# Kernel optimization log

Hardware: AMD Instinct MI355X
Metric: run time of the kernel (lower is better)

## Reference

```python
import jax, jax.numpy as jnp
import numpy as np

B, N, K = 16, 8192, 16
H1, H3 = 512, 64
EPS = 1e-5


def _bn(x, g, b):
    # BatchNorm1d training-mode math: normalize per-channel (last axis) over all other axes.
    ax = tuple(range(x.ndim - 1))
    m = x.mean(ax, keepdims=True)
    v = x.var(ax, keepdims=True)  # biased variance, as in torch BN forward
    return (x - m) * jax.lax.rsqrt(v + EPS) * g + b


def _gather(h, idx):
    # h: [b,n,f], idx: [b,n,k] -> [b,n,k,f] per-batch neighbor gather
    return jax.vmap(lambda hb, ib: hb[ib])(h, idx)


def _forward(data, knn, e1_w, e1_b, e1_g, e1_be,
             gc1_w, gc1_b, g1_g, g1_be, gc2_w, gc2_b, g2_g, g2_be,
             e2_w, e2_b, e2_g, e2_be,
             d1_w, d1_b, d1_g, d1_be, d2_w, d2_b, d2_g, d2_be):
    b, n, _ = data.shape
    # local covariance features
    neigh = _gather(data, knn)                       # [b,n,K,3]
    cen = neigh - neigh.mean(axis=2, keepdims=True)
    cov = jnp.einsum('bnki,bnkj->bnij', cen, cen) / (K - 1)
    x = jnp.concatenate([data, cov.reshape(b, n, 9)], axis=-1)  # [b,n,12]
    # e_layers1: Linear(12,h3) + BN + ReLU
    x = jax.nn.relu(_bn(x @ e1_w + e1_b, e1_g, e1_be))
    # GCNConv over uniform-degree kNN graph with self loop: (h_i + sum_j h_j)/(K+1)
    deg = float(K + 1)
    h = x @ gc1_w
    h = (h + _gather(h, knn).sum(axis=2)) / deg + gc1_b
    x = jax.nn.relu(_bn(h, g1_g, g1_be))
    h = x @ gc2_w
    h = (h + _gather(h, knn).sum(axis=2)) / deg + gc2_b
    x = jax.nn.relu(_bn(h, g2_g, g2_be))             # [b,n,h1]
    # AdaptiveMaxPool1d(1) over nodes
    x = x.max(axis=1, keepdims=True)                 # [b,1,h1]
    # e_layers2: Linear(h1,h1) + BN + ReLU
    x = jax.nn.relu(_bn(x @ e2_w + e2_b, e2_g, e2_be))
    # decode: folding grid
    nx_ = int(1 + (n * 120 / 60) ** 0.5)
    ny_ = int(1 + (n * 60 / 120) ** 0.5)
    xg = jnp.linspace(1.0, 120.0, nx_)
    yg = jnp.linspace(1.0, 60.0, ny_)
    grid = jnp.stack(jnp.meshgrid(xg, yg, indexing='ij'), axis=-1).reshape(-1, 2)[:n]
    kfeat = jnp.broadcast_to(x, (b, n, x.shape[-1]))  # codeword repeated per node
    y = jnp.broadcast_to(grid[None], (b, n, 2))
    z = jnp.concatenate([kfeat, y], axis=-1)          # [b,n,h1+2]
    z = jax.nn.relu(_bn(z @ d1_w + d1_b, d1_g, d1_be))
    z = jnp.concatenate([kfeat, z], axis=-1)          # [b,n,h1+3]
    z = jax.nn.relu(_bn(z @ d2_w + d2_b, d2_g, d2_be))
    return z                                          # [b,n,3]


def setup_inputs() -> dict:
    key = jax.random.key(0)
    ks = jax.random.split(key, 8)

    def lin(k, i, o):
        s = 1.0 / np.sqrt(i)
        return jax.random.uniform(k, (i, o), jnp.float32, -s, s)

    ones = lambda c: jnp.ones((c,), jnp.float32)
    zeros = lambda c: jnp.zeros((c,), jnp.float32)
    return {
        'data': jax.random.normal(ks[0], (B, N, 3), jnp.float32),
        'knn': jax.random.randint(ks[1], (B, N, K), 0, N),
        'e1_w': lin(ks[2], 12, H3), 'e1_b': zeros(H3), 'e1_g': ones(H3), 'e1_be': zeros(H3),
        'gc1_w': lin(ks[3], H3, 2 * H3), 'gc1_b': zeros(2 * H3), 'g1_g': ones(2 * H3), 'g1_be': zeros(2 * H3),
        'gc2_w': lin(ks[4], 2 * H3, H1), 'gc2_b': zeros(H1), 'g2_g': ones(H1), 'g2_be': zeros(H1),
        'e2_w': lin(ks[5], H1, H1), 'e2_b': zeros(H1), 'e2_g': ones(H1), 'e2_be': zeros(H1),
        'd1_w': lin(ks[6], H1 + 2, 3), 'd1_b': zeros(3), 'd1_g': ones(3), 'd1_be': zeros(3),
        'd2_w': lin(ks[7], H1 + 3, 3), 'd2_b': zeros(3), 'd2_g': ones(3), 'd2_be': zeros(3),
    }


def reference(data, knn, e1_w, e1_b, e1_g, e1_be,
              gc1_w, gc1_b, g1_g, g1_be, gc2_w, gc2_b, g2_g, g2_be,
              e2_w, e2_b, e2_g, e2_be,
              d1_w, d1_b, d1_g, d1_be, d2_w, d2_b, d2_g, d2_be):
    return _forward(data, knn, e1_w, e1_b, e1_g, e1_be,
                    gc1_w, gc1_b, g1_g, g1_be, gc2_w, gc2_b, g2_g, g2_be,
                    e2_w, e2_b, e2_g, e2_be,
                    d1_w, d1_b, d1_g, d1_be, d2_w, d2_b, d2_g, d2_be)
```

## Files before the change

kernel.cpp:

```cpp
#include <hip/hip_runtime.h>
#include <hip/hip_fp16.h>
#include <stdint.h>

#define BATCH 16
#define NPTS  8192
#define KNN   16
#define NROWS (BATCH*NPTS)
#define EPSBN 1e-5f
#define DEGINV (1.0f/17.0f)

typedef _Float16 f16x8 __attribute__((ext_vector_type(8)));
typedef float    f32x4 __attribute__((ext_vector_type(4)));

__device__ __forceinline__ unsigned short f2hu(float f) {
    union { _Float16 h; unsigned short u; } cv;
    cv.h = (_Float16)f;
    return cv.u;
}
__device__ __forceinline__ float hu2f(unsigned short u) {
    union { unsigned short u; _Float16 h; } cv;
    cv.u = u;
    return (float)cv.h;
}
__device__ __forceinline__ unsigned fenc(float f) {
    unsigned u = __float_as_uint(f);
    return (int)u >= 0 ? (u | 0x80000000u) : ~u;
}
__device__ __forceinline__ float fdec(unsigned k) {
    return (k & 0x80000000u) ? __uint_as_float(k & 0x7FFFFFFFu) : __uint_as_float(~k);
}

#define SZ_S1    0
#define SZ_S2P   128
#define SZ_S3P   16512
#define SZ_S4    82048
#define SZ_C1    83072
#define SZ_GN    83080
#define SZ_D2    83088
#define SZ_SCSH1 83096
#define SZ_SCSH2 83224
#define SZ_TOT   83480

__global__ __launch_bounds__(256) void k_prep(
    const float* __restrict__ gc1w, const float* __restrict__ gc2w,
    const float* __restrict__ d1w, const float* __restrict__ d1b,
    unsigned short* __restrict__ W1T, unsigned short* __restrict__ W2T,
    float* __restrict__ gn, float* __restrict__ statszone, unsigned* __restrict__ mm)
{
    int t = blockIdx.x * 256 + threadIdx.x;
    int NT_ = gridDim.x * 256;
    for (int i = t; i < 65536; i += NT_) {
        int c = i >> 7, k = i & 127;
        W2T[i] = f2hu(gc2w[k * 512 + c]);
    }
    for (int i = t; i < 8192; i += NT_) {
        int c = i >> 6, k = i & 63;
        W1T[i] = f2hu(gc1w[k * 128 + c]);
    }
    for (int i = t; i < SZ_TOT; i += NT_) statszone[i] = 0.f;
    for (int i = t; i < 8192; i += NT_) mm[i] = 0u;
    for (int i = t; i < 8192; i += NT_) mm[8192 + i] = 0xFFFFFFFFu;
    for (int n = t; n < 8192; n += NT_) {
        int ix = n / 65, iy = n % 65;
        float gx = 1.f + ix * (119.f / 128.f);
        float gy = 1.f + iy * (59.f / 64.f);
        #pragma unroll
        for (int j = 0; j < 3; j++)
            gn[n * 3 + j] = gx * d1w[512 * 3 + j] + gy * d1w[513 * 3 + j] + d1b[j];
    }
}

__global__ __launch_bounds__(256) void k_cov_e1(
    const float* __restrict__ data, const int* __restrict__ knn,
    const float* __restrict__ e1w, const float* __restrict__ e1b,
    unsigned short* __restrict__ a1)
{
    __shared__ float w[12 * 64];
    __shared__ float bias[64];
    int tid = threadIdx.x;
    for (int i = tid; i < 768; i += 256) w[i] = e1w[i];
    if (tid < 64) bias[tid] = e1b[tid];
    __syncthreads();

    int gid = blockIdx.x * 256 + tid;
    int b = gid >> 13;
    const float* db = data + (size_t)b * NPTS * 3;
    const int4* k4 = (const int4*)knn + gid * 4;

    float sx = 0, sy = 0, sz = 0, Sxx = 0, Sxy = 0, Sxz = 0, Syy = 0, Syz = 0, Szz = 0;
    #pragma unroll
    for (int jj = 0; jj < 4; jj++) {
        int4 q = k4[jj];
        int id[4] = {q.x, q.y, q.z, q.w};
        #pragma unroll
        for (int u = 0; u < 4; u++) {
            const float* p = db + (size_t)id[u] * 3;
            float x = p[0], y = p[1], z = p[2];
            sx += x; sy += y; sz += z;
            Sxx += x * x; Sxy += x * y; Sxz += x * z;
            Syy += y * y; Syz += y * z; Szz += z * z;
        }
    }
    float mx = sx * (1.f / 16.f), my = sy * (1.f / 16.f), mz = sz * (1.f / 16.f);
    const float inv15 = 1.f / 15.f;
    float x12[12];
    x12[0] = data[(size_t)gid * 3 + 0];
    x12[1] = data[(size_t)gid * 3 + 1];
    x12[2] = data[(size_t)gid * 3 + 2];
    x12[3] = (Sxx - 16.f * mx * mx) * inv15;
    x12[4] = (Sxy - 16.f * mx * my) * inv15;
    x12[5] = (Sxz - 16.f * mx * mz) * inv15;
    x12[6] = x12[4];
    x12[7] = (Syy - 16.f * my * my) * inv15;
    x12[8] = (Syz - 16.f * my * mz) * inv15;
    x12[9] = x12[5];
    x12[10] = x12[8];
    x12[11] = (Szz - 16.f * mz * mz) * inv15;

    unsigned short* arow = a1 + (size_t)gid * 64;
    for (int c0 = 0; c0 < 64; c0 += 8) {
        float v8[8];
        #pragma unroll
        for (int u = 0; u < 8; u++) {
            int c = c0 + u;
            float acc = bias[c];
            #pragma unroll
            for (int i = 0; i < 12; i++) acc += x12[i] * w[i * 64 + c];
            v8[u] = acc;
        }
        uint4 o;
        o.x = f2hu(v8[0]) | ((unsigned)f2hu(v8[1]) << 16);
        o.y = f2hu(v8[2]) | ((unsigned)f2hu(v8[3]) << 16);
        o.z = f2hu(v8[4]) | ((unsigned)f2hu(v8[5]) << 16);
        o.w = f2hu(v8[6]) | ((unsigned)f2hu(v8[7]) << 16);
        *(uint4*)(arow + c0) = o;
    }
}

__global__ __launch_bounds__(256) void k_reduce_a1(
    const unsigned short* __restrict__ a1, float* __restrict__ stats1)
{
    int tid = threadIdx.x;
    int c = tid & 63, rq = tid >> 6;
    float s = 0.f, q = 0.f;
    for (int row = blockIdx.x * 4 + rq; row < NROWS; row += gridDim.x * 4) {
        float v = hu2f(a1[(size_t)row * 64 + c]);
        s += v; q += v * v;
    }
    __shared__ float red[2][256];
    red[0][tid] = s; red[1][tid] = q;
    __syncthreads();
    if (tid < 64) {
        s = red[0][tid] + red[0][tid + 64] + red[0][tid + 128] + red[0][tid + 192];
        q = red[1][tid] + red[1][tid + 64] + red[1][tid + 128] + red[1][tid + 192];
        atomicAdd(stats1 + tid, s);
        atomicAdd(stats1 + 64 + tid, q);
    }
}

template <int C, int NPARTS>
__global__ __launch_bounds__(256) void k_bncoef(
    const float* __restrict__ statsIn,
    const float* __restrict__ gamma, const float* __restrict__ beta,
    float* __restrict__ scsh)
{
    int ch = threadIdx.x;
    if (ch < C) {
        float s = 0.f, q = 0.f;
        for (int p = 0; p < NPARTS; p++) {
            s += statsIn[p * 2 * C + ch];
            q += statsIn[p * 2 * C + C + ch];
        }
        float m = s * (1.f / NROWS);
        float var = fmaxf(q * (1.f / NROWS) - m * m, 0.f);
        float sc = gamma[ch] * rsqrtf(var + EPSBN);
        scsh[ch] = sc;
        scsh[C + ch] = beta[ch] - m * sc;
    }
}

template <int CIN>
__global__ __launch_bounds__(256) void k_gather16(
    const unsigned short* __restrict__ ain, const int* __restrict__ knn,
    const float* __restrict__ scsh, unsigned short* __restrict__ S)
{
    constexpr int GPR = CIN / 8;
    constexpr int R = 256 / GPR;
    constexpr int R2 = 2 * R;
    constexpr int BPB = NPTS / R2;

    __shared__ int nidx[R2 * KNN];

    int tid = threadIdx.x;
    int blk = blockIdx.x;
    int xcd = blk & 7;
    int idx = blk >> 3;
    int batch = xcd + 8 * (idx / BPB);
    int within = idx % BPB;
    int node0 = batch * NPTS + within * R2;

    {
        const int4* ksrc = (const int4*)(knn + (size_t)node0 * KNN);
        for (int i = tid; i < R2 * 4; i += 256) ((int4*)nidx)[i] = ksrc[i];
    }
    __syncthreads();

    int t = tid & (GPR - 1);
    int r0 = tid / GPR;
    int col8 = t * 8;
    float sc8[8], sh8[8];
    #pragma unroll
    for (int j = 0; j < 8; j++) { sc8[j] = scsh[col8 + j]; sh8[j] = scsh[CIN + col8 + j]; }

    int ra = node0 + r0;
    int rb = node0 + r0 + R;
    const unsigned short* abase = ain + (size_t)batch * NPTS * CIN;

    float acca[8], accb[8];
    {
        uint4 va = *(const uint4*)(ain + (size_t)ra * CIN + col8);
        uint4 vb = *(const uint4*)(ain + (size_t)rb * CIN + col8);
        unsigned wa[4] = {va.x, va.y, va.z, va.w};
        unsigned wb[4] = {vb.x, vb.y, vb.z, vb.w};
        #pragma unroll
        for (int j = 0; j < 4; j++) {
            acca[2*j]   = fmaxf(hu2f((unsigned short)(wa[j] & 0xFFFF)) * sc8[2*j]   + sh8[2*j],   0.f);
            acca[2*j+1] = fmaxf(hu2f((unsigned short)(wa[j] >> 16))    * sc8[2*j+1] + sh8[2*j+1], 0.f);
            accb[2*j]   = fmaxf(hu2f((unsigned short)(wb[j] & 0xFFFF)) * sc8[2*j]   + sh8[2*j],   0.f);
            accb[2*j+1] = fmaxf(hu2f((unsigned short)(wb[j] >> 16))    * sc8[2*j+1] + sh8[2*j+1], 0.f);
        }
    }
    #pragma unroll
    for (int jn = 0; jn < KNN; jn++) {
        int sa = nidx[r0 * KNN + jn];
        int sb = nidx[(r0 + R) * KNN + jn];
        uint4 va = *(const uint4*)(abase + (size_t)sa * CIN + col8);
        uint4 vb = *(const uint4*)(abase + (size_t)sb * CIN + col8);
        unsigned wa[4] = {va.x, va.y, va.z, va.w};
        unsigned wb[4] = {vb.x, vb.y, vb.z, vb.w};
        #pragma unroll
        for (int j = 0; j < 4; j++) {
            acca[2*j]   += fmaxf(hu2f((unsigned short)(wa[j] & 0xFFFF)) * sc8[2*j]   + sh8[2*j],   0.f);
            acca[2*j+1] += fmaxf(hu2f((unsigned short)(wa[j] >> 16))    * sc8[2*j+1] + sh8[2*j+1], 0.f);
            accb[2*j]   += fmaxf(hu2f((unsigned short)(wb[j] & 0xFFFF)) * sc8[2*j]   + sh8[2*j],   0.f);
            accb[2*j+1] += fmaxf(hu2f((unsigned short)(wb[j] >> 16))    * sc8[2*j+1] + sh8[2*j+1], 0.f);
        }
    }
    uint4 oa, ob;
    oa.x = f2hu(acca[0]) | ((unsigned)f2hu(acca[1]) << 16);
    oa.y = f2hu(acca[2]) | ((unsigned)f2hu(acca[3]) << 16);
    oa.z = f2hu(acca[4]) | ((unsigned)f2hu(acca[5]) << 16);
    oa.w = f2hu(acca[6]) | ((unsigned)f2hu(acca[7]) << 16);
    ob.x = f2hu(accb[0]) | ((unsigned)f2hu(accb[1]) << 16);
    ob.y = f2hu(accb[2]) | ((unsigned)f2hu(accb[3]) << 16);
    ob.z = f2hu(accb[4]) | ((unsigned)f2hu(accb[5]) << 16);
    ob.w = f2hu(accb[6]) | ((unsigned)f2hu(accb[7]) << 16);
    *(uint4*)(S + (size_t)ra * CIN + col8) = oa;
    *(uint4*)(S + (size_t)rb * CIN + col8) = ob;
}

template <int CIN, int COUT, int NSPLIT, bool STORE>
__global__ __launch_bounds__(256) void k_gemm(
    const unsigned short* __restrict__ S, const unsigned short* __restrict__ WT,
    const float* __restrict__ bias,
    unsigned short* __restrict__ aout, float* __restrict__ statsOut, unsigned* __restrict__ mm)
{
    constexpr int KC = CIN / 32;
    constexpr int MT = 128;
    constexpr int SST = CIN + 8;
    constexpr int CPB = COUT / NSPLIT;
    constexpr int CPW = CPB / 4;
    constexpr int NT = CPW / 16;

    __shared__ alignas(16) unsigned short sA[MT * SST];

    int tid = threadIdx.x;
    int blk = blockIdx.x;
    int xcd = blk & 7;
    int rest = blk >> 3;
    int nq = rest % NSPLIT;
    int mseq = rest / NSPLIT;
    int phase = mseq >> 6;
    int within = mseq & 63;
    int batch = xcd + 8 * phase;
    int node0 = batch * NPTS + within * MT;
    int cbase = nq * CPB;
    int pout = batch * 4 + (within >> 4);

    {
        constexpr int TOT = MT * CIN / 8;
        const uint4* src = (const uint4*)(S + (size_t)node0 * CIN);
        #pragma unroll
        for (int i = tid; i < TOT; i += 256) {
            int row = i / (CIN / 8);
            int col8 = (i % (CIN / 8)) * 8;
            *(uint4*)&sA[row * SST + col8] = src[i];
        }
    }
    __syncthreads();

    int lane = tid & 63, wv = tid >> 6;
    int n15 = lane & 15, qd = lane >> 4;
    int c0 = cbase + wv * CPW;

    f16x8 wf[KC][NT];
    float bz[NT];
    #pragma unroll
    for (int nt = 0; nt < NT; nt++) {
        int c = c0 + nt * 16 + n15;
        bz[nt] = bias[c];
        #pragma unroll
        for (int kc = 0; kc < KC; kc++)
            wf[kc][nt] = *(const f16x8*)(WT + (size_t)c * CIN + kc * 32 + qd * 8);
    }
    float sacc[NT], qacc[NT], mxa[NT], mna[NT];
    #pragma unroll
    for (int nt = 0; nt < NT; nt++) {
        sacc[nt] = 0.f; qacc[nt] = 0.f; mxa[nt] = -3.4e38f; mna[nt] = 3.4e38f;
    }

    #pragma unroll
    for (int mt = 0; mt < MT / 16; mt++) {
        f16x8 af[KC];
        #pragma unroll
        for (int kc = 0; kc < KC; kc++)
            af[kc] = *(const f16x8*)&sA[(mt * 16 + n15) * SST + kc * 32 + qd * 8];

        f32x4 acc[NT];
        #pragma unroll
        for (int nt = 0; nt < NT; nt++) acc[nt] = (f32x4)(0.f);
        #pragma unroll
        for (int kc = 0; kc < KC; kc++)
            #pragma unroll
            for (int nt = 0; nt < NT; nt++)
                acc[nt] = __builtin_amdgcn_mfma_f32_16x16x32_f16(af[kc], wf[kc][nt], acc[nt], 0, 0, 0);

        #pragma unroll
        for (int nt = 0; nt < NT; nt++) {
            int c = c0 + nt * 16 + n15;
            #pragma unroll
            for (int r = 0; r < 4; r++) {
                float a = acc[nt][r];
                sacc[nt] += a;
                qacc[nt] = fmaf(a, a, qacc[nt]);
                if (!STORE) {
                    mxa[nt] = fmaxf(mxa[nt], a);
                    mna[nt] = fminf(mna[nt], a);
                }
                if (STORE) {
                    float v = a * DEGINV + bz[nt];
                    int node = node0 + mt * 16 + qd * 4 + r;
                    aout[(size_t)node * COUT + c] = f2hu(v);
                }
            }
        }
    }

    #pragma unroll
    for (int nt = 0; nt < NT; nt++) {
        int c = c0 + nt * 16 + n15;
        float S_ = sacc[nt], Q_ = qacc[nt];
        S_ += __shfl_xor(S_, 16); S_ += __shfl_xor(S_, 32);
        Q_ += __shfl_xor(Q_, 16); Q_ += __shfl_xor(Q_, 32);
        if (!STORE) {
            float mx = mxa[nt], mn = mna[nt];
            mx = fmaxf(mx, __shfl_xor(mx, 16)); mx = fmaxf(mx, __shfl_xor(mx, 32));
            mn = fminf(mn, __shfl_xor(mn, 16)); mn = fminf(mn, __shfl_xor(mn, 32));
            if (lane < 16) {
                atomicMax(mm + batch * COUT + c, fenc(mx * DEGINV + bz[nt]));
                atomicMin(mm + BATCH * COUT + batch * COUT + c, fenc(mn * DEGINV + bz[nt]));
            }
        }
        if (lane < 16) {
            float b = bz[nt];
            float s = DEGINV * S_ + (float)MT * b;
            float q = DEGINV * DEGINV * Q_ + 2.f * DEGINV * b * S_ + (float)MT * b * b;
            atomicAdd(statsOut + (size_t)pout * 2 * COUT + c, s);
            atomicAdd(statsOut + (size_t)pout * 2 * COUT + COUT + c, q);
        }
    }
}

__global__ __launch_bounds__(256) void k_e2(
    const float* __restrict__ stats3p, const unsigned* __restrict__ mm,
    const float* __restrict__ g2g, const float* __restrict__ g2be,
    const float* __restrict__ e2w, const float* __restrict__ e2b,
    float* __restrict__ a4, float* __restrict__ stats4)
{
    __shared__ float pooled[512];
    int b = blockIdx.x, tid = threadIdx.x;
    for (int c = tid; c < 512; c += 256) {
        float s = 0.f, qq = 0.f;
        for (int p = 0; p < 64; p++) {
            s += stats3p[p * 1024 + c];
            qq += stats3p[p * 1024 + 512 + c];
        }
        float m = s * (1.f / NROWS);
        float var = fmaxf(qq * (1.f / NROWS) - m * m, 0.f);
        float sc = g2g[c] * rsqrtf(var + EPSBN);
        float sh = g2be[c] - m * sc;
        float amax = fdec(mm[b * 512 + c]);
        float amin = fdec(mm[8192 + b * 512 + c]);
        pooled[c] = fmaxf(fmaxf(sc * amax + sh, 0.f), fmaxf(sc * amin + sh, 0.f));
    }
    __syncthreads();
    int ca = tid, cb = tid + 256;
    float acc1 = e2b[ca], acc2 = e2b[cb];
    for (int f = 0; f < 512; f++) {
        float pv = pooled[f];
        acc1 += pv * e2w[f * 512 + ca];
        acc2 += pv * e2w[f * 512 + cb];
    }
    a4[b * 512 + ca] = acc1; a4[b * 512 + cb] = acc2;
    atomicAdd(stats4 + ca, acc1); atomicAdd(stats4 + 512 + ca, acc1 * acc1);
    atomicAdd(stats4 + cb, acc2); atomicAdd(stats4 + 512 + cb, acc2 * acc2);
}

__global__ __launch_bounds__(256) void k_code(
    const float* __restrict__ a4, const float* __restrict__ stats4,
    const float* __restrict__ e2g, const float* __restrict__ e2be,
    const float* __restrict__ d1w, const float* __restrict__ d2w,
    const float* __restrict__ gn,
    float* __restrict__ c1, float* __restrict__ c2,
    float* __restrict__ c1stats, float* __restrict__ gnstats)
{
    int b = blockIdx.x, tid = threadIdx.x;
    int lane = tid & 63, wv = tid >> 6;
    float p1[3] = {0, 0, 0}, p2[3] = {0, 0, 0};
    for (int c = tid; c < 512; c += 256) {
        float s = stats4[c], qq = stats4[512 + c];
        float m = s * (1.f / 16.f);
        float var = fmaxf(qq * (1.f / 16.f) - m * m, 0.f);
        float sc = e2g[c] * rsqrtf(var + EPSBN);
        float sh = e2be[c] - m * sc;
        float cv = fmaxf(sc * a4[b * 512 + c] + sh, 0.f);
        #pragma unroll
        for (int j = 0; j < 3; j++) {
            p1[j] += cv * d1w[c * 3 + j];
            p2[j] += cv * d2w[c * 3 + j];
        }
    }
    __shared__ float red[4][6];
    #pragma unroll
    for (int j = 0; j < 3; j++)
        for (int off = 32; off; off >>= 1) {
            p1[j] += __shfl_xor(p1[j], off);
            p2[j] += __shfl_xor(p2[j], off);
        }
    if (lane == 0) {
        #pragma unroll
        for (int j = 0; j < 3; j++) { red[wv][j] = p1[j]; red[wv][3 + j] = p2[j]; }
    }
    __syncthreads();
    if (tid < 3) {
        float v = red[0][tid] + red[1][tid] + red[2][tid] + red[3][tid];
        c1[b * 3 + tid] = v;
        atomicAdd(c1stats + tid, v);
        atomicAdd(c1stats + 3 + tid, v * v);
    } else if (tid < 6) {
        int j = tid - 3;
        float v = red[0][tid] + red[1][tid] + red[2][tid] + red[3][tid];
        c2[b * 3 + j] = v;
    }
    if (blockIdx.x == 0) {
        float g1[3] = {0, 0, 0}, g2s[3] = {0, 0, 0};
        for (int n = tid; n < NPTS; n += 256) {
            #pragma unroll
            for (int j = 0; j < 3; j++) {
                float g = gn[n * 3 + j];
                g1[j] += g; g2s[j] += g * g;
            }
        }
        #pragma unroll
        for (int j = 0; j < 3; j++)
            for (int off = 32; off; off >>= 1) {
                g1[j] += __shfl_xor(g1[j], off);
                g2s[j] += __shfl_xor(g2s[j], off);
            }
        __shared__ float redg[4][6];
        if (lane == 0) {
            #pragma unroll
            for (int j = 0; j < 3; j++) { redg[wv][j] = g1[j]; redg[wv][3 + j] = g2s[j]; }
        }
        __syncthreads();
        if (tid < 6)
            gnstats[tid] = redg[0][tid] + redg[1][tid] + redg[2][tid] + redg[3][tid];
    }
}

__device__ __forceinline__ void d1_coefs(
    const float* c1stats, const float* gnstats,
    const float* d1g, const float* d1be, float* scd, float* shd)
{
    #pragma unroll
    for (int j = 0; j < 3; j++) {
        float mc = c1stats[j] * (1.f / 16.f), qc = c1stats[3 + j] * (1.f / 16.f);
        float mg = gnstats[j] * (1.f / 8192.f), qg = gnstats[3 + j] * (1.f / 8192.f);
        float m = mc + mg;
        float var = fmaxf((qc - mc * mc) + (qg - mg * mg), 0.f);
        float sc = d1g[j] * rsqrtf(var + EPSBN);
        scd[j] = sc;
        shd[j] = d1be[j] - m * sc;
    }
}

__global__ __launch_bounds__(256) void k_d2stats(
    const float* __restrict__ c1, const float* __restrict__ c2, const float* __restrict__ gn,
    const float* __restrict__ c1stats, const float* __restrict__ gnstats,
    const float* __restrict__ d1g, const float* __restrict__ d1be,
    const float* __restrict__ d2w, const float* __restrict__ d2b,
    float* __restrict__ statsd2)
{
    int gid = blockIdx.x * 256 + threadIdx.x;
    int b = gid >> 13, n = gid & 8191;
    int lane = threadIdx.x & 63, wv = threadIdx.x >> 6;
    float scd[3], shd[3];
    d1_coefs(c1stats, gnstats, d1g, d1be, scd, shd);
    float z3[3];
    #pragma unroll
    for (int j = 0; j < 3; j++)
        z3[j] = fmaxf(scd[j] * (c1[b * 3 + j] + gn[n * 3 + j]) + shd[j], 0.f);
    float vals[6];
    #pragma unroll
    for (int u = 0; u < 3; u++) {
        float a = c2[b * 3 + u]
                + z3[0] * d2w[512 * 3 + u]
                + z3[1] * d2w[513 * 3 + u]
                + z3[2] * d2w[514 * 3 + u]
                + d2b[u];
        vals[u] = a; vals[3 + u] = a * a;
    }
    #pragma unroll
    for (int j = 0; j < 6; j++)
        for (int off = 32; off; off >>= 1) vals[j] += __shfl_xor(vals[j], off);
    __shared__ float red[4][6];
    if (lane == 0) {
        #pragma unroll
        for (int j = 0; j < 6; j++) red[wv][j] = vals[j];
    }
    __syncthreads();
    if (threadIdx.x < 6)
        atomicAdd(statsd2 + threadIdx.x,
                  red[0][threadIdx.x] + red[1][threadIdx.x] + red[2][threadIdx.x] + red[3][threadIdx.x]);
}

__global__ __launch_bounds__(256) void k_out(
    const float* __restrict__ c1, const float* __restrict__ c2, const float* __restrict__ gn,
    const float* __restrict__ c1stats, const float* __restrict__ gnstats,
    const float* __restrict__ statsd2,
    const float* __restrict__ d1g, const float* __restrict__ d1be,
    const float* __restrict__ d2w, const float* __restrict__ d2b,
    const float* __restrict__ d2g, const float* __restrict__ d2be,
    float* __restrict__ out)
{
    int gid = blockIdx.x * 256 + threadIdx.x;
    int b = gid >> 13, n = gid & 8191;
    float scd[3], shd[3];
    d1_coefs(c1stats, gnstats, d1g, d1be, scd, shd);
    float z3[3];
    #pragma unroll
    for (int j = 0; j < 3; j++)
        z3[j] = fmaxf(scd[j] * (c1[b * 3 + j] + gn[n * 3 + j]) + shd[j], 0.f);
    #pragma unroll
    for (int u = 0; u < 3; u++) {
        float a = c2[b * 3 + u]
                + z3[0] * d2w[512 * 3 + u]
                + z3[1] * d2w[513 * 3 + u]
                + z3[2] * d2w[514 * 3 + u]
                + d2b[u];
        float m2 = statsd2[u] * (1.f / (float)NROWS);
        float v2 = fmaxf(statsd2[3 + u] * (1.f / (float)NROWS) - m2 * m2, 0.f);
        float sc = d2g[u] * rsqrtf(v2 + EPSBN);
        float sh = d2be[u] - m2 * sc;
        out[(size_t)gid * 3 + u] = fmaxf(sc * a + sh, 0.f);
    }
}

extern "C" void kernel_launch(void* const* d_in, const int* in_sizes, int n_in,
                              void* d_out, int out_size, void* d_ws, size_t ws_size,
                              hipStream_t stream)
{
    (void)in_sizes; (void)n_in; (void)out_size; (void)ws_size;
    const float* data = (const float*)d_in[0];
    const int*   knn  = (const int*)d_in[1];
    const float* e1w = (const float*)d_in[2],  *e1b = (const float*)d_in[3];
    const float* e1g = (const float*)d_in[4],  *e1be = (const float*)d_in[5];
    const float* gc1w = (const float*)d_in[6], *gc1b = (const float*)d_in[7];
    const float* g1g = (const float*)d_in[8],  *g1be = (const float*)d_in[9];
    const float* gc2w = (const float*)d_in[10], *gc2b = (const float*)d_in[11];
    const float* g2g = (const float*)d_in[12], *g2be = (const float*)d_in[13];
    const float* e2w = (const float*)d_in[14], *e2b = (const float*)d_in[15];
    const float* e2g = (const float*)d_in[16], *e2be = (const float*)d_in[17];
    const float* d1w = (const float*)d_in[18], *d1b = (const float*)d_in[19];
    const float* d1g = (const float*)d_in[20], *d1be = (const float*)d_in[21];
    const float* d2w = (const float*)d_in[22], *d2b = (const float*)d_in[23];
    const float* d2g = (const float*)d_in[24], *d2be = (const float*)d_in[25];

    char* p = (char*)d_ws;
    auto alloc = [&](size_t bytes) -> void* {
        void* r = (void*)p;
        p += (bytes + 255) & ~(size_t)255;
        return r;
    };
    unsigned short* a1  = (unsigned short*)alloc((size_t)NROWS * 64 * 2);
    unsigned short* a2h = (unsigned short*)alloc((size_t)NROWS * 128 * 2);
    unsigned short* s1  = (unsigned short*)alloc((size_t)NROWS * 64 * 2);
    unsigned short* s2  = (unsigned short*)alloc((size_t)NROWS * 128 * 2);
    unsigned short* W1T = (unsigned short*)alloc(8192 * 2);
    unsigned short* W2T = (unsigned short*)alloc(65536 * 2);
    float* statszone = (float*)alloc(SZ_TOT * 4);
    float* stats1  = statszone + SZ_S1;
    float* stats2p = statszone + SZ_S2P;
    float* stats3p = statszone + SZ_S3P;
    float* stats4  = statszone + SZ_S4;
    float* c1stats = statszone + SZ_C1;
    float* gnstats = statszone + SZ_GN;
    float* statsd2 = statszone + SZ_D2;
    float* scsh1   = statszone + SZ_SCSH1;
    float* scsh2   = statszone + SZ_SCSH2;
    unsigned* mm = (unsigned*)alloc(16384 * 4);
    float* a4 = (float*)alloc(16 * 512 * 4);
    float* c1 = (float*)alloc(64 * 4);
    float* c2 = (float*)alloc(64 * 4);
    float* gn = (float*)alloc(8192 * 3 * 4);

    k_prep<<<64, 256, 0, stream>>>(gc1w, gc2w, d1w, d1b, W1T, W2T, gn, statszone, mm);
    k_cov_e1<<<512, 256, 0, stream>>>(data, knn, e1w, e1b, a1);
    k_reduce_a1<<<256, 256, 0, stream>>>(a1, stats1);
    k_bncoef<64, 1><<<1, 256, 0, stream>>>(stats1, e1g, e1be, scsh1);
    k_gather16<64><<<NROWS / 64, 256, 0, stream>>>(a1, knn, scsh1, s1);
    k_gemm<64, 128, 1, true><<<1024, 256, 0, stream>>>(s1, W1T, gc1b, a2h, stats2p, nullptr);
    k_bncoef<128, 64><<<1, 256, 0, stream>>>(stats2p, g1g, g1be, scsh2);
    k_gather16<128><<<NROWS / 32, 256, 0, stream>>>(a2h, knn, scsh2, s2);
    k_gemm<128, 512, 4, false><<<4096, 256, 0, stream>>>(s2, W2T, gc2b, nullptr, stats3p, mm);
    k_e2<<<16, 256, 0, stream>>>(stats3p, mm, g2g, g2be, e2w, e2b, a4, stats4);
    k_code<<<16, 256, 0, stream>>>(a4, stats4, e2g, e2be, d1w, d2w, gn, c1, c2, c1stats, gnstats);
    k_d2stats<<<512, 256, 0, stream>>>(c1, c2, gn, c1stats, gnstats, d1g, d1be, d2w, d2b, statsd2);
    k_out<<<512, 256, 0, stream>>>(c1, c2, gn, c1stats, gnstats, statsd2,
                                   d1g, d1be, d2w, d2b, d2g, d2be, (float*)d_out);
}
```

Measured before the change: 341.8 us.

## Pad point data to float4 for gathers and split e2 GEMV across more blocks

```diff
diff --git a/kernel.cpp b/kernel.cpp
--- a/kernel.cpp
+++ b/kernel.cpp
@@ -42,10 +42,12 @@
 #define SZ_TOT   83480
 
 __global__ __launch_bounds__(256) void k_prep(
-    const float* __restrict__ gc1w, const float* __restrict__ gc2w,
+    const float* __restrict__ data, const float* __restrict__ gc1w,
+    const float* __restrict__ gc2w,
     const float* __restrict__ d1w, const float* __restrict__ d1b,
     unsigned short* __restrict__ W1T, unsigned short* __restrict__ W2T,
-    float* __restrict__ gn, float* __restrict__ statszone, unsigned* __restrict__ mm)
+    float* __restrict__ gn, float* __restrict__ statszone, unsigned* __restrict__ mm,
+    float4* __restrict__ data4)
 {
     int t = blockIdx.x * 256 + threadIdx.x;
     int NT_ = gridDim.x * 256;
@@ -60,6 +62,14 @@
     for (int i = t; i < SZ_TOT; i += NT_) statszone[i] = 0.f;
     for (int i = t; i < 8192; i += NT_) mm[i] = 0u;
     for (int i = t; i < 8192; i += NT_) mm[8192 + i] = 0xFFFFFFFFu;
+    for (int i = t; i < NROWS; i += NT_) {
+        float4 v;
+        v.x = data[(size_t)i * 3 + 0];
+        v.y = data[(size_t)i * 3 + 1];
+        v.z = data[(size_t)i * 3 + 2];
+        v.w = 0.f;
+        data4[i] = v;
+    }
     for (int n = t; n < 8192; n += NT_) {
         int ix = n / 65, iy = n % 65;
         float gx = 1.f + ix * (119.f / 128.f);
@@ -71,7 +81,7 @@
 }
 
 __global__ __launch_bounds__(256) void k_cov_e1(
-    const float* __restrict__ data, const int* __restrict__ knn,
+    const float4* __restrict__ data4, const int* __restrict__ knn,
     const float* __restrict__ e1w, const float* __restrict__ e1b,
     unsigned short* __restrict__ a1)
 {
@@ -84,7 +94,7 @@
 
     int gid = blockIdx.x * 256 + tid;
     int b = gid >> 13;
-    const float* db = data + (size_t)b * NPTS * 3;
+    const float4* db4 = data4 + (size_t)b * NPTS;
     const int4* k4 = (const int4*)knn + gid * 4;
 
     float sx = 0, sy = 0, sz = 0, Sxx = 0, Sxy = 0, Sxz = 0, Syy = 0, Syz = 0, Szz = 0;
@@ -94,8 +104,8 @@
         int id[4] = {q.x, q.y, q.z, q.w};
         #pragma unroll
         for (int u = 0; u < 4; u++) {
-            const float* p = db + (size_t)id[u] * 3;
-            float x = p[0], y = p[1], z = p[2];
+            float4 p = db4[id[u]];
+            float x = p.x, y = p.y, z = p.z;
             sx += x; sy += y; sz += z;
             Sxx += x * x; Sxy += x * y; Sxz += x * z;
             Syy += y * y; Syz += y * z; Szz += z * z;
@@ -103,10 +113,11 @@
     }
     float mx = sx * (1.f / 16.f), my = sy * (1.f / 16.f), mz = sz * (1.f / 16.f);
     const float inv15 = 1.f / 15.f;
+    float4 self = data4[gid];
     float x12[12];
-    x12[0] = data[(size_t)gid * 3 + 0];
-    x12[1] = data[(size_t)gid * 3 + 1];
-    x12[2] = data[(size_t)gid * 3 + 2];
+    x12[0] = self.x;
+    x12[1] = self.y;
+    x12[2] = self.z;
     x12[3] = (Sxx - 16.f * mx * mx) * inv15;
     x12[4] = (Sxy - 16.f * mx * my) * inv15;
     x12[5] = (Sxz - 16.f * mx * mz) * inv15;
@@ -381,13 +392,11 @@
     }
 }
 
-__global__ __launch_bounds__(256) void k_e2(
+__global__ __launch_bounds__(256) void k_pool(
     const float* __restrict__ stats3p, const unsigned* __restrict__ mm,
     const float* __restrict__ g2g, const float* __restrict__ g2be,
-    const float* __restrict__ e2w, const float* __restrict__ e2b,
-    float* __restrict__ a4, float* __restrict__ stats4)
-{
-    __shared__ float pooled[512];
+    float* __restrict__ pooledg)
+{
     int b = blockIdx.x, tid = threadIdx.x;
     for (int c = tid; c < 512; c += 256) {
         float s = 0.f, qq = 0.f;
@@ -401,19 +410,38 @@
         float sh = g2be[c] - m * sc;
         float amax = fdec(mm[b * 512 + c]);
         float amin = fdec(mm[8192 + b * 512 + c]);
-        pooled[c] = fmaxf(fmaxf(sc * amax + sh, 0.f), fmaxf(sc * amin + sh, 0.f));
-    }
-    __syncthreads();
-    int ca = tid, cb = tid + 256;
-    float acc1 = e2b[ca], acc2 = e2b[cb];
-    for (int f = 0; f < 512; f++) {
-        float pv = pooled[f];
-        acc1 += pv * e2w[f * 512 + ca];
-        acc2 += pv * e2w[f * 512 + cb];
-    }
-    a4[b * 512 + ca] = acc1; a4[b * 512 + cb] = acc2;
-    atomicAdd(stats4 + ca, acc1); atomicAdd(stats4 + 512 + ca, acc1 * acc1);
-    atomicAdd(stats4 + cb, acc2); atomicAdd(stats4 + 512 + cb, acc2 * acc2);
+        pooledg[b * 512 + c] = fmaxf(fmaxf(sc * amax + sh, 0.f), fmaxf(sc * amin + sh, 0.f));
+    }
+}
+
+__global__ __launch_bounds__(256) void k_e2(
+    const float* __restrict__ pooledg,
+    const float* __restrict__ e2w, const float* __restrict__ e2b,
+    float* __restrict__ a4, float* __restrict__ stats4)
+{
+    __shared__ float pooled[512];
+    __shared__ float red[4][64];
+    int blk = blockIdx.x;
+    int b = blk >> 3, cg = blk & 7;
+    int tid = threadIdx.x;
+    for (int i = tid; i < 512; i += 256) pooled[i] = pooledg[b * 512 + i];
+    __syncthreads();
+
+    int c = cg * 64 + (tid & 63);
+    int fg = tid >> 6;
+    float acc = 0.f;
+    #pragma unroll 4
+    for (int f = fg * 128; f < fg * 128 + 128; f++)
+        acc += pooled[f] * e2w[(size_t)f * 512 + c];
+    red[fg][tid & 63] = acc;
+    __syncthreads();
+    if (tid < 64) {
+        int cc = cg * 64 + tid;
+        float v = red[0][tid] + red[1][tid] + red[2][tid] + red[3][tid] + e2b[cc];
+        a4[b * 512 + cc] = v;
+        atomicAdd(stats4 + cc, v);
+        atomicAdd(stats4 + 512 + cc, v * v);
+    }
 }
 
 __global__ __launch_bounds__(256) void k_code(
@@ -606,6 +634,7 @@
     unsigned short* a2h = (unsigned short*)alloc((size_t)NROWS * 128 * 2);
     unsigned short* s1  = (unsigned short*)alloc((size_t)NROWS * 64 * 2);
     unsigned short* s2  = (unsigned short*)alloc((size_t)NROWS * 128 * 2);
+    float4* data4 = (float4*)alloc((size_t)NROWS * 16);
     unsigned short* W1T = (unsigned short*)alloc(8192 * 2);
     unsigned short* W2T = (unsigned short*)alloc(65536 * 2);
     float* statszone = (float*)alloc(SZ_TOT * 4);
@@ -620,12 +649,14 @@
     float* scsh2   = statszone + SZ_SCSH2;
     unsigned* mm = (unsigned*)alloc(16384 * 4);
     float* a4 = (float*)alloc(16 * 512 * 4);
+    float* pooledg = (float*)alloc(16 * 512 * 4);
     float* c1 = (float*)alloc(64 * 4);
     float* c2 = (float*)alloc(64 * 4);
     float* gn = (float*)alloc(8192 * 3 * 4);
 
-    k_prep<<<64, 256, 0, stream>>>(gc1w, gc2w, d1w, d1b, W1T, W2T, gn, statszone, mm);
-    k_cov_e1<<<512, 256, 0, stream>>>(data, knn, e1w, e1b, a1);
+    k_prep<<<128, 256, 0, stream>>>(data, gc1w, gc2w, d1w, d1b, W1T, W2T, gn,
+                                    statszone, mm, data4);
+    k_cov_e1<<<512, 256, 0, stream>>>(data4, knn, e1w, e1b, a1);
     k_reduce_a1<<<256, 256, 0, stream>>>(a1, stats1);
     k_bncoef<64, 1><<<1, 256, 0, stream>>>(stats1, e1g, e1be, scsh1);
     k_gather16<64><<<NROWS / 64, 256, 0, stream>>>(a1, knn, scsh1, s1);
@@ -633,7 +664,8 @@
     k_bncoef<128, 64><<<1, 256, 0, stream>>>(stats2p, g1g, g1be, scsh2);
     k_gather16<128><<<NROWS / 32, 256, 0, stream>>>(a2h, knn, scsh2, s2);
     k_gemm<128, 512, 4, false><<<4096, 256, 0, stream>>>(s2, W2T, gc2b, nullptr, stats3p, mm);
-    k_e2<<<16, 256, 0, stream>>>(stats3p, mm, g2g, g2be, e2w, e2b, a4, stats4);
+    k_pool<<<16, 256, 0, stream>>>(stats3p, mm, g2g, g2be, pooledg);
+    k_e2<<<128, 256, 0, stream>>>(pooledg, e2w, e2b, a4, stats4);
     k_code<<<16, 256, 0, stream>>>(a4, stats4, e2g, e2be, d1w, d2w, gn, c1, c2, c1stats, gnstats);
     k_d2stats<<<512, 256, 0, stream>>>(c1, c2, gn, c1stats, gnstats, d1g, d1be, d2w, d2b, statsd2);
     k_out<<<512, 256, 0, stream>>>(c1, c2, gn, c1stats, gnstats, statsd2,
```

New measurement: 331.3 us. -3.1%, faster.
